# Kernel optimization log

Hardware: AMD Instinct MI355X
Metric: run time of the kernel (lower is better)

The kernel has to match this reference:

```python
import jax, jax.numpy as jnp
import numpy as np

H = 4  # num_heads
EPS = 1e-5


def setup_inputs() -> dict:
    key = jax.random.key(0)
    ks = jax.random.split(key, 12)
    N, C, E = 4096, 128, 131072
    x = jax.random.normal(ks[0], (N, C), dtype=jnp.float32)
    edge_index = jax.random.randint(ks[1], (2, E), 0, N, dtype=jnp.int64)
    # guarantee every row has at least one neighbor (self-loops) to avoid NaN softmax rows
    loops = jnp.arange(N, dtype=jnp.int64)
    edge_index = edge_index.at[0, :N].set(loops).at[1, :N].set(loops)
    s = 1.0 / np.sqrt(C)
    def lin(k):
        kw, kb = jax.random.split(k)
        return (jax.random.uniform(kw, (C, C), jnp.float32, -s, s),
                jax.random.uniform(kb, (C,), jnp.float32, -s, s))
    wq, bq = lin(ks[2]); wk, bk = lin(ks[3]); wv, bv = lin(ks[4]); wo, bo = lin(ks[5])
    gamma = jnp.ones((C,), jnp.float32)
    beta = jnp.zeros((C,), jnp.float32)
    return {"x": x, "edge_index": edge_index, "wq": wq, "bq": bq, "wk": wk, "bk": bk,
            "wv": wv, "bv": bv, "wo": wo, "bo": bo, "gamma": gamma, "beta": beta}


def reference(x, edge_index, wq, bq, wk, bk, wv, bv, wo, bo, gamma, beta):
    N, C = x.shape
    D = C // H
    q = (x @ wq.T + bq).reshape(N, H, D)
    k = (x @ wk.T + bk).reshape(N, H, D)
    v = (x @ wv.T + bv).reshape(N, H, D)
    scores = jnp.einsum('nhd,mhd->nhm', q, k) / jnp.sqrt(jnp.float32(D))  # [N,H,N]
    row, col = edge_index
    mask = jnp.zeros((N, N), jnp.float32).at[row, col].set(1.0)
    scores = jnp.where(mask[:, None, :] == 0, -jnp.inf, scores)
    attn = jax.nn.softmax(scores, axis=-1)  # dropout is identity in eval
    out = jnp.einsum('nhm,mhd->nhd', attn, v).reshape(N, C)
    out = out @ wo.T + bo
    y = x + out
    mu = jnp.mean(y, axis=-1, keepdims=True)
    var = jnp.var(y, axis=-1, keepdims=True)
    return (y - mu) / jnp.sqrt(var + EPS) * gamma + beta
```

## Files before the change

kernel.cpp:

```cpp
#include <hip/hip_runtime.h>

typedef unsigned long long u64;
typedef unsigned short u16;
typedef __attribute__((ext_vector_type(8))) short short8;
typedef __attribute__((ext_vector_type(4))) float f32x4;

#define C_DIM 128

__device__ inline u16 bf16_rn(float f) {
    unsigned u = __float_as_uint(f);
    u += 0x7FFF + ((u >> 16) & 1);
    return (u16)(u >> 16);
}
__device__ inline float bf16_tof(u16 h) { return __uint_as_float(((unsigned)h) << 16); }

__global__ __launch_bounds__(256) void prep_kernel(
    const int* __restrict__ ei, int E, u64* __restrict__ bm, int wpr,
    const float* __restrict__ x, u16* __restrict__ xh, u16* __restrict__ xl, int xq,
    const float* __restrict__ wq, const float* __restrict__ wk,
    const float* __restrict__ wv, const float* __restrict__ wo,
    u16* __restrict__ wH, u16* __restrict__ wL)
{
    int tid = blockIdx.x * 256 + threadIdx.x;
    if (tid < E) {
        int r = ei[tid], c = ei[E + tid];
        atomicOr(&bm[(size_t)r * wpr + (c >> 6)], 1ull << (c & 63));
    }
    if (tid < 4 * C_DIM * C_DIM) {
        int s = tid >> 14, i = tid & 16383;
        const float* W = (s == 0) ? wq : (s == 1) ? wk : (s == 2) ? wv : wo;
        float f = W[i];
        u16 h = bf16_rn(f);
        wH[tid] = h;
        wL[tid] = bf16_rn(f - bf16_tof(h));
    }
    if (tid < xq) {
        float4 xv = ((const float4*)x)[tid];
        ushort4 h, l;
        h.x = bf16_rn(xv.x); l.x = bf16_rn(xv.x - bf16_tof(h.x));
        h.y = bf16_rn(xv.y); l.y = bf16_rn(xv.y - bf16_tof(h.y));
        h.z = bf16_rn(xv.z); l.z = bf16_rn(xv.z - bf16_tof(h.z));
        h.w = bf16_rn(xv.w); l.w = bf16_rn(xv.w - bf16_tof(h.w));
        ((ushort4*)xh)[tid] = h;
        ((ushort4*)xl)[tid] = l;
    }
}

__global__ __launch_bounds__(256) void qkv_mfma_kernel(
    const u16* __restrict__ xh, const u16* __restrict__ xl,
    const u16* __restrict__ wH, const u16* __restrict__ wL,
    const float* __restrict__ bq, const float* __restrict__ bk, const float* __restrict__ bv,
    float* __restrict__ qo, float* __restrict__ ko, float* __restrict__ vo, int nrg)
{
    int bid = blockIdx.x;
    int s = bid / nrg;
    int rg = bid % nrg;
    int r0 = rg * 16;
    int w  = threadIdx.x >> 6;
    int l  = threadIdx.x & 63;
    int j0 = w * 32;
    int lr = l & 15;
    int kg = l >> 4;

    const u16* xhp = xh + (size_t)(r0 + lr) * C_DIM + kg * 8;
    const u16* xlp = xl + (size_t)(r0 + lr) * C_DIM + kg * 8;
    const u16* wh  = wH + (size_t)s * C_DIM * C_DIM;
    const u16* wl  = wL + (size_t)s * C_DIM * C_DIM;
    const u16* w0h = wh + (size_t)(j0 + lr) * C_DIM + kg * 8;
    const u16* w0l = wl + (size_t)(j0 + lr) * C_DIM + kg * 8;
    const u16* w1h = w0h + 16 * C_DIM;
    const u16* w1l = w0l + 16 * C_DIM;
    const float* B = (s == 0) ? bq : (s == 1) ? bk : bv;
    float*       O = (s == 0) ? qo : (s == 1) ? ko : vo;
    float fin = (s == 0) ? 0.17677669529663687f : 1.0f;

    float b0 = B[j0 + lr], b1 = B[j0 + 16 + lr];
    f32x4 acc0 = {b0, b0, b0, b0};
    f32x4 acc1 = {b1, b1, b1, b1};

    #pragma unroll
    for (int kk = 0; kk < C_DIM; kk += 32) {
        short8 ah  = *(const short8*)(xhp + kk);
        short8 al  = *(const short8*)(xlp + kk);
        short8 bh0 = *(const short8*)(w0h + kk);
        short8 bl0 = *(const short8*)(w0l + kk);
        short8 bh1 = *(const short8*)(w1h + kk);
        short8 bl1 = *(const short8*)(w1l + kk);
        acc0 = __builtin_amdgcn_mfma_f32_16x16x32_bf16(ah, bh0, acc0, 0, 0, 0);
        acc0 = __builtin_amdgcn_mfma_f32_16x16x32_bf16(ah, bl0, acc0, 0, 0, 0);
        acc0 = __builtin_amdgcn_mfma_f32_16x16x32_bf16(al, bh0, acc0, 0, 0, 0);
        acc1 = __builtin_amdgcn_mfma_f32_16x16x32_bf16(ah, bh1, acc1, 0, 0, 0);
        acc1 = __builtin_amdgcn_mfma_f32_16x16x32_bf16(ah, bl1, acc1, 0, 0, 0);
        acc1 = __builtin_amdgcn_mfma_f32_16x16x32_bf16(al, bh1, acc1, 0, 0, 0);
    }
    size_t ob = (size_t)(r0 + kg * 4) * C_DIM;
    #pragma unroll
    for (int i = 0; i < 4; ++i) {
        O[ob + (size_t)i * C_DIM + j0 + lr]      = acc0[i] * fin;
        O[ob + (size_t)i * C_DIM + j0 + 16 + lr] = acc1[i] * fin;
    }
}

__global__ __launch_bounds__(512, 4) void attn_kernel(
    const float* __restrict__ q, const float* __restrict__ k,
    const float* __restrict__ v, const u64* __restrict__ bm, int wpr,
    u16* __restrict__ aoh, u16* __restrict__ aol)
{
    __shared__ int lm[8][64];
    int t = threadIdx.x;
    int wave = t >> 6, lane = t & 63;
    int n = blockIdx.x * 8 + wave;

    u64 bits = bm[(size_t)n * wpr + lane];
    int pc = __popcll(bits);
    int incl = pc;
    #pragma unroll
    for (int off = 1; off < 64; off <<= 1) {
        int tv = __shfl_up(incl, off);
        if (lane >= off) incl += tv;
    }
    int cnt = __builtin_amdgcn_readfirstlane(__shfl(incl, 63));
    int pos = incl - pc;
    u64 bb = bits;
    while (bb) {
        int b = __builtin_ctzll(bb);
        bb &= bb - 1;
        if (pos < 64) lm[wave][pos] = (lane << 6) + b;
        ++pos;
    }
    if (cnt > 64) cnt = 64;

    int g = lane >> 4;
    float2 qf = *(const float2*)(q + (size_t)n * C_DIM + 2 * lane);

    float sc0 = -1e30f, sc1 = -1e30f, sc2 = -1e30f, sc3 = -1e30f;
    float2 buf[32];

    {
        int top = cnt < 32 ? cnt : 32;
        #pragma unroll
        for (int u = 0; u < 32; ++u)
            if (u < top)
                buf[u] = *(const float2*)(k + (size_t)lm[wave][u] * C_DIM + 2 * lane);
        #pragma unroll
        for (int u = 0; u < 32; ++u)
            if (u < top) {
                float s = qf.x * buf[u].x + qf.y * buf[u].y;
                s += __shfl_xor(s, 1); s += __shfl_xor(s, 2);
                s += __shfl_xor(s, 4); s += __shfl_xor(s, 8);
                if ((lane & 15) == (u & 15)) { if (u < 16) sc0 = s; else sc1 = s; }
            }
    }
    if (cnt > 32) {
        #pragma unroll
        for (int u = 0; u < 32; ++u)
            if (32 + u < cnt)
                buf[u] = *(const float2*)(k + (size_t)lm[wave][32 + u] * C_DIM + 2 * lane);
        #pragma unroll
        for (int u = 0; u < 32; ++u)
            if (32 + u < cnt) {
                float s = qf.x * buf[u].x + qf.y * buf[u].y;
                s += __shfl_xor(s, 1); s += __shfl_xor(s, 2);
                s += __shfl_xor(s, 4); s += __shfl_xor(s, 8);
                if ((lane & 15) == (u & 15)) { if (u < 16) sc2 = s; else sc3 = s; }
            }
    }
    {
        int top = cnt < 32 ? cnt : 32;
        #pragma unroll
        for (int u = 0; u < 32; ++u)
            if (u < top)
                buf[u] = *(const float2*)(v + (size_t)lm[wave][u] * C_DIM + 2 * lane);
    }
    float mx = fmaxf(fmaxf(sc0, sc1), fmaxf(sc2, sc3));
    mx = fmaxf(mx, __shfl_xor(mx, 1)); mx = fmaxf(mx, __shfl_xor(mx, 2));
    mx = fmaxf(mx, __shfl_xor(mx, 4)); mx = fmaxf(mx, __shfl_xor(mx, 8));
    float e0 = __expf(sc0 - mx), e1 = __expf(sc1 - mx);
    float e2 = __expf(sc2 - mx), e3 = __expf(sc3 - mx);
    float sum = (e0 + e1) + (e2 + e3);
    sum += __shfl_xor(sum, 1); sum += __shfl_xor(sum, 2);
    sum += __shfl_xor(sum, 4); sum += __shfl_xor(sum, 8);
    float sinv = 1.0f / sum;

    float2 acc = {0.f, 0.f};
    {
        int top = cnt < 32 ? cnt : 32;
        #pragma unroll
        for (int u = 0; u < 32; ++u)
            if (u < top) {
                float e = __shfl((u < 16) ? e0 : e1, (g << 4) | (u & 15));
                acc.x += e * buf[u].x;
                acc.y += e * buf[u].y;
            }
    }
    if (cnt > 32) {
        #pragma unroll
        for (int u = 0; u < 32; ++u)
            if (32 + u < cnt)
                buf[u] = *(const float2*)(v + (size_t)lm[wave][32 + u] * C_DIM + 2 * lane);
        #pragma unroll
        for (int u = 0; u < 32; ++u)
            if (32 + u < cnt) {
                float e = __shfl((u < 16) ? e2 : e3, (g << 4) | (u & 15));
                acc.x += e * buf[u].x;
                acc.y += e * buf[u].y;
            }
    }
    float f0 = acc.x * sinv, f1 = acc.y * sinv;
    ushort2 ho, lo;
    ho.x = bf16_rn(f0); lo.x = bf16_rn(f0 - bf16_tof(ho.x));
    ho.y = bf16_rn(f1); lo.y = bf16_rn(f1 - bf16_tof(ho.y));
    *(ushort2*)(aoh + (size_t)n * C_DIM + 2 * lane) = ho;
    *(ushort2*)(aol + (size_t)n * C_DIM + 2 * lane) = lo;
}

__global__ __launch_bounds__(256) void oln_kernel(
    const u16* __restrict__ aoh, const u16* __restrict__ aol,
    const u16* __restrict__ woh, const u16* __restrict__ wol,
    const float* __restrict__ bo, const float* __restrict__ x,
    const float* __restrict__ gamma, const float* __restrict__ beta,
    float* __restrict__ out)
{
    __shared__ float ys[16 * 132];
    int r0 = blockIdx.x * 16;
    int w  = threadIdx.x >> 6;
    int l  = threadIdx.x & 63;
    int j0 = w * 32;
    int lr = l & 15;
    int kg = l >> 4;

    const u16* ahp = aoh + (size_t)(r0 + lr) * C_DIM + kg * 8;
    const u16* alp = aol + (size_t)(r0 + lr) * C_DIM + kg * 8;
    const u16* w0h = woh + (size_t)(j0 + lr) * C_DIM + kg * 8;
    const u16* w0l = wol + (size_t)(j0 + lr) * C_DIM + kg * 8;
    const u16* w1h = w0h + 16 * C_DIM;
    const u16* w1l = w0l + 16 * C_DIM;

    float b0 = bo[j0 + lr], b1 = bo[j0 + 16 + lr];
    f32x4 acc0 = {b0, b0, b0, b0};
    f32x4 acc1 = {b1, b1, b1, b1};

    #pragma unroll
    for (int kk = 0; kk < C_DIM; kk += 32) {
        short8 ah  = *(const short8*)(ahp + kk);
        short8 al  = *(const short8*)(alp + kk);
        short8 bh0 = *(const short8*)(w0h + kk);
        short8 bl0 = *(const short8*)(w0l + kk);
        short8 bh1 = *(const short8*)(w1h + kk);
        short8 bl1 = *(const short8*)(w1l + kk);
        acc0 = __builtin_amdgcn_mfma_f32_16x16x32_bf16(ah, bh0, acc0, 0, 0, 0);
        acc0 = __builtin_amdgcn_mfma_f32_16x16x32_bf16(ah, bl0, acc0, 0, 0, 0);
        acc0 = __builtin_amdgcn_mfma_f32_16x16x32_bf16(al, bh0, acc0, 0, 0, 0);
        acc1 = __builtin_amdgcn_mfma_f32_16x16x32_bf16(ah, bh1, acc1, 0, 0, 0);
        acc1 = __builtin_amdgcn_mfma_f32_16x16x32_bf16(ah, bl1, acc1, 0, 0, 0);
        acc1 = __builtin_amdgcn_mfma_f32_16x16x32_bf16(al, bh1, acc1, 0, 0, 0);
    }
    #pragma unroll
    for (int i = 0; i < 4; ++i) {
        int rr = kg * 4 + i;
        float y0 = acc0[i] + x[(size_t)(r0 + rr) * C_DIM + j0 + lr];
        float y1 = acc1[i] + x[(size_t)(r0 + rr) * C_DIM + j0 + 16 + lr];
        ys[rr * 132 + j0 + lr]      = y0;
        ys[rr * 132 + j0 + 16 + lr] = y1;
    }
    __syncthreads();
    {
        int rr = threadIdx.x >> 4;
        int c0 = (threadIdx.x & 15) * 8;
        float yv[8];
        float s = 0.f, s2 = 0.f;
        #pragma unroll
        for (int u = 0; u < 8; ++u) {
            yv[u] = ys[rr * 132 + c0 + u];
            s += yv[u]; s2 += yv[u] * yv[u];
        }
        #pragma unroll
        for (int off = 8; off; off >>= 1) {
            s  += __shfl_xor(s, off);
            s2 += __shfl_xor(s2, off);
        }
        float mu = s * (1.0f / 128.0f);
        float var = s2 * (1.0f / 128.0f) - mu * mu;
        float rstd = rsqrtf(var + 1e-5f);
        size_t o = (size_t)(r0 + rr) * C_DIM + c0;
        #pragma unroll
        for (int u = 0; u < 8; ++u)
            out[o + u] = (yv[u] - mu) * rstd * gamma[c0 + u] + beta[c0 + u];
    }
}

extern "C" void kernel_launch(void* const* d_in, const int* in_sizes, int n_in,
                              void* d_out, int out_size, void* d_ws, size_t ws_size,
                              hipStream_t stream)
{
    const float* x     = (const float*)d_in[0];
    const int*   ei    = (const int*)d_in[1];
    const float* wq    = (const float*)d_in[2];
    const float* bq    = (const float*)d_in[3];
    const float* wk    = (const float*)d_in[4];
    const float* bk    = (const float*)d_in[5];
    const float* wv    = (const float*)d_in[6];
    const float* bv    = (const float*)d_in[7];
    const float* wo    = (const float*)d_in[8];
    const float* bo    = (const float*)d_in[9];
    const float* gamma = (const float*)d_in[10];
    const float* beta  = (const float*)d_in[11];
    float* out = (float*)d_out;

    int N = in_sizes[0] / C_DIM;
    int E = in_sizes[1] / 2;
    int wpr = N >> 6;

    size_t MB = 1 << 20;
    char* base = (char*)d_ws;
    float* q   = (float*)(base + 0 * MB);
    float* k   = (float*)(base + 2 * MB);
    float* v   = (float*)(base + 4 * MB);
    u64*   bm  = (u64*)(base + 6 * MB);
    u16*   xh  = (u16*)(base + 8 * MB);
    u16*   xl  = (u16*)(base + 9 * MB);
    u16*   wH  = (u16*)(base + 10 * MB);
    u16*   wL  = (u16*)(base + 10 * MB + 512 * 1024);
    u16*   aoh = (u16*)(base + 11 * MB);
    u16*   aol = (u16*)(base + 12 * MB);

    hipMemsetAsync(bm, 0, (size_t)N * wpr * sizeof(u64), stream);

    int xq = N * C_DIM / 4;
    int nwork = (E > xq) ? E : xq;
    prep_kernel<<<(nwork + 255) / 256, 256, 0, stream>>>(
        ei, E, bm, wpr, x, xh, xl, xq, wq, wk, wv, wo, wH, wL);

    int nrg = N / 16;
    qkv_mfma_kernel<<<3 * nrg, 256, 0, stream>>>(
        xh, xl, wH, wL, bq, bk, bv, q, k, v, nrg);

    attn_kernel<<<N / 8, 512, 0, stream>>>(q, k, v, bm, wpr, aoh, aol);

    oln_kernel<<<N / 16, 256, 0, stream>>>(
        aoh, aol, wH + 3 * C_DIM * C_DIM, wL + 3 * C_DIM * C_DIM,
        bo, x, gamma, beta, out);
}
```

Baseline: 125.5 us.

## Build neighbor lists during prep and double row tiles in QKV and output GEMMs

The prep kernel now appends each unique neighbor to a per-row list with an atomic degree counter whenever the bitmap atomicOr sets a new bit. The attention kernel then reads the list directly instead of doing popcount, prefix scan and LDS compaction. The weight split conversion is vectorized with float4. QKV and output-projection kernels now compute 32 rows per block instead of 16, which halves the grid and reuses the weight fragments. The costs are extra atomics in prep, a list order that depends on atomic timing, and fewer blocks in the GEMM kernels.

New measurement: 137.4 us. 9.5% more time.

```diff
diff --git a/kernel.cpp b/kernel.cpp
--- a/kernel.cpp
+++ b/kernel.cpp
@@ -16,6 +16,7 @@
 
 __global__ __launch_bounds__(256) void prep_kernel(
     const int* __restrict__ ei, int E, u64* __restrict__ bm, int wpr,
+    int* __restrict__ deg, u16* __restrict__ lists,
     const float* __restrict__ x, u16* __restrict__ xh, u16* __restrict__ xl, int xq,
     const float* __restrict__ wq, const float* __restrict__ wk,
     const float* __restrict__ wv, const float* __restrict__ wo,
@@ -24,15 +25,24 @@
     int tid = blockIdx.x * 256 + threadIdx.x;
     if (tid < E) {
         int r = ei[tid], c = ei[E + tid];
-        atomicOr(&bm[(size_t)r * wpr + (c >> 6)], 1ull << (c & 63));
-    }
-    if (tid < 4 * C_DIM * C_DIM) {
-        int s = tid >> 14, i = tid & 16383;
+        u64 mask = 1ull << (c & 63);
+        u64 old = atomicOr(&bm[(size_t)r * wpr + (c >> 6)], mask);
+        if (!(old & mask)) {
+            int slot = atomicAdd(&deg[r], 1);
+            if (slot < 64) lists[(size_t)r * 64 + slot] = (u16)c;
+        }
+    }
+    if (tid < 4 * 4096) {
+        int s = tid >> 12, i4 = tid & 4095;
         const float* W = (s == 0) ? wq : (s == 1) ? wk : (s == 2) ? wv : wo;
-        float f = W[i];
-        u16 h = bf16_rn(f);
-        wH[tid] = h;
-        wL[tid] = bf16_rn(f - bf16_tof(h));
+        float4 f = ((const float4*)W)[i4];
+        ushort4 h, l;
+        h.x = bf16_rn(f.x); l.x = bf16_rn(f.x - bf16_tof(h.x));
+        h.y = bf16_rn(f.y); l.y = bf16_rn(f.y - bf16_tof(h.y));
+        h.z = bf16_rn(f.z); l.z = bf16_rn(f.z - bf16_tof(h.z));
+        h.w = bf16_rn(f.w); l.w = bf16_rn(f.w - bf16_tof(h.w));
+        ((ushort4*)(wH + (size_t)s * 16384))[i4] = h;
+        ((ushort4*)(wL + (size_t)s * 16384))[i4] = l;
     }
     if (tid < xq) {
         float4 xv = ((const float4*)x)[tid];
@@ -55,19 +65,19 @@
     int bid = blockIdx.x;
     int s = bid / nrg;
     int rg = bid % nrg;
-    int r0 = rg * 16;
+    int r0 = rg * 32;
     int w  = threadIdx.x >> 6;
     int l  = threadIdx.x & 63;
     int j0 = w * 32;
     int lr = l & 15;
     int kg = l >> 4;
 
-    const u16* xhp = xh + (size_t)(r0 + lr) * C_DIM + kg * 8;
-    const u16* xlp = xl + (size_t)(r0 + lr) * C_DIM + kg * 8;
-    const u16* wh  = wH + (size_t)s * C_DIM * C_DIM;
-    const u16* wl  = wL + (size_t)s * C_DIM * C_DIM;
-    const u16* w0h = wh + (size_t)(j0 + lr) * C_DIM + kg * 8;
-    const u16* w0l = wl + (size_t)(j0 + lr) * C_DIM + kg * 8;
+    const u16* a0h = xh + (size_t)(r0 + lr) * C_DIM + kg * 8;
+    const u16* a0l = xl + (size_t)(r0 + lr) * C_DIM + kg * 8;
+    const u16* a1h = a0h + 16 * C_DIM;
+    const u16* a1l = a0l + 16 * C_DIM;
+    const u16* w0h = wH + (size_t)s * 16384 + (size_t)(j0 + lr) * C_DIM + kg * 8;
+    const u16* w0l = wL + (size_t)s * 16384 + (size_t)(j0 + lr) * C_DIM + kg * 8;
     const u16* w1h = w0h + 16 * C_DIM;
     const u16* w1l = w0l + 16 * C_DIM;
     const float* B = (s == 0) ? bq : (s == 1) ? bk : bv;
@@ -75,60 +85,59 @@
     float fin = (s == 0) ? 0.17677669529663687f : 1.0f;
 
     float b0 = B[j0 + lr], b1 = B[j0 + 16 + lr];
-    f32x4 acc0 = {b0, b0, b0, b0};
-    f32x4 acc1 = {b1, b1, b1, b1};
+    f32x4 acc00 = {b0, b0, b0, b0};
+    f32x4 acc01 = {b1, b1, b1, b1};
+    f32x4 acc10 = {b0, b0, b0, b0};
+    f32x4 acc11 = {b1, b1, b1, b1};
 
     #pragma unroll
     for (int kk = 0; kk < C_DIM; kk += 32) {
-        short8 ah  = *(const short8*)(xhp + kk);
-        short8 al  = *(const short8*)(xlp + kk);
+        short8 ah0 = *(const short8*)(a0h + kk);
+        short8 al0 = *(const short8*)(a0l + kk);
+        short8 ah1 = *(const short8*)(a1h + kk);
+        short8 al1 = *(const short8*)(a1l + kk);
         short8 bh0 = *(const short8*)(w0h + kk);
         short8 bl0 = *(const short8*)(w0l + kk);
         short8 bh1 = *(const short8*)(w1h + kk);
         short8 bl1 = *(const short8*)(w1l + kk);
-        acc0 = __builtin_amdgcn_mfma_f32_16x16x32_bf16(ah, bh0, acc0, 0, 0, 0);
-        acc0 = __builtin_amdgcn_mfma_f32_16x16x32_bf16(ah, bl0, acc0, 0, 0, 0);
-        acc0 = __builtin_amdgcn_mfma_f32_16x16x32_bf16(al, bh0, acc0, 0, 0, 0);
-        acc1 = __builtin_amdgcn_mfma_f32_16x16x32_bf16(ah, bh1, acc1, 0, 0, 0);
-        acc1 = __builtin_amdgcn_mfma_f32_16x16x32_bf16(ah, bl1, acc1, 0, 0, 0);
-        acc1 = __builtin_amdgcn_mfma_f32_16x16x32_bf16(al, bh1, acc1, 0, 0, 0);
-    }
-    size_t ob = (size_t)(r0 + kg * 4) * C_DIM;
+        acc00 = __builtin_amdgcn_mfma_f32_16x16x32_bf16(ah0, bh0, acc00, 0, 0, 0);
+        acc00 = __builtin_amdgcn_mfma_f32_16x16x32_bf16(ah0, bl0, acc00, 0, 0, 0);
+        acc00 = __builtin_amdgcn_mfma_f32_16x16x32_bf16(al0, bh0, acc00, 0, 0, 0);
+        acc01 = __builtin_amdgcn_mfma_f32_16x16x32_bf16(ah0, bh1, acc01, 0, 0, 0);
+        acc01 = __builtin_amdgcn_mfma_f32_16x16x32_bf16(ah0, bl1, acc01, 0, 0, 0);
+        acc01 = __builtin_amdgcn_mfma_f32_16x16x32_bf16(al0, bh1, acc01, 0, 0, 0);
+        acc10 = __builtin_amdgcn_mfma_f32_16x16x32_bf16(ah1, bh0, acc10, 0, 0, 0);
+        acc10 = __builtin_amdgcn_mfma_f32_16x16x32_bf16(ah1, bl0, acc10, 0, 0, 0);
+        acc10 = __builtin_amdgcn_mfma_f32_16x16x32_bf16(al1, bh0, acc10, 0, 0, 0);
+        acc11 = __builtin_amdgcn_mfma_f32_16x16x32_bf16(ah1, bh1, acc11, 0, 0, 0);
+        acc11 = __builtin_amdgcn_mfma_f32_16x16x32_bf16(ah1, bl1, acc11, 0, 0, 0);
+        acc11 = __builtin_amdgcn_mfma_f32_16x16x32_bf16(al1, bh1, acc11, 0, 0, 0);
+    }
     #pragma unroll
     for (int i = 0; i < 4; ++i) {
-        O[ob + (size_t)i * C_DIM + j0 + lr]      = acc0[i] * fin;
-        O[ob + (size_t)i * C_DIM + j0 + 16 + lr] = acc1[i] * fin;
+        size_t ro0 = (size_t)(r0 + kg * 4 + i) * C_DIM;
+        size_t ro1 = (size_t)(r0 + 16 + kg * 4 + i) * C_DIM;
+        O[ro0 + j0 + lr]      = acc00[i] * fin;
+        O[ro0 + j0 + 16 + lr] = acc01[i] * fin;
+        O[ro1 + j0 + lr]      = acc10[i] * fin;
+        O[ro1 + j0 + 16 + lr] = acc11[i] * fin;
     }
 }
 
 __global__ __launch_bounds__(512, 4) void attn_kernel(
     const float* __restrict__ q, const float* __restrict__ k,
-    const float* __restrict__ v, const u64* __restrict__ bm, int wpr,
+    const float* __restrict__ v, const int* __restrict__ deg,
+    const u16* __restrict__ lists,
     u16* __restrict__ aoh, u16* __restrict__ aol)
 {
-    __shared__ int lm[8][64];
     int t = threadIdx.x;
     int wave = t >> 6, lane = t & 63;
     int n = blockIdx.x * 8 + wave;
 
-    u64 bits = bm[(size_t)n * wpr + lane];
-    int pc = __popcll(bits);
-    int incl = pc;
-    #pragma unroll
-    for (int off = 1; off < 64; off <<= 1) {
-        int tv = __shfl_up(incl, off);
-        if (lane >= off) incl += tv;
-    }
-    int cnt = __builtin_amdgcn_readfirstlane(__shfl(incl, 63));
-    int pos = incl - pc;
-    u64 bb = bits;
-    while (bb) {
-        int b = __builtin_ctzll(bb);
-        bb &= bb - 1;
-        if (pos < 64) lm[wave][pos] = (lane << 6) + b;
-        ++pos;
-    }
+    int cnt = deg[n];
     if (cnt > 64) cnt = 64;
+    cnt = __builtin_amdgcn_readfirstlane(cnt);
+    int le = lists[(size_t)n * 64 + lane];
 
     int g = lane >> 4;
     float2 qf = *(const float2*)(q + (size_t)n * C_DIM + 2 * lane);
@@ -140,8 +149,10 @@
         int top = cnt < 32 ? cnt : 32;
         #pragma unroll
         for (int u = 0; u < 32; ++u)
-            if (u < top)
-                buf[u] = *(const float2*)(k + (size_t)lm[wave][u] * C_DIM + 2 * lane);
+            if (u < top) {
+                int m = __shfl(le, u);
+                buf[u] = *(const float2*)(k + (size_t)m * C_DIM + 2 * lane);
+            }
         #pragma unroll
         for (int u = 0; u < 32; ++u)
             if (u < top) {
@@ -154,8 +165,10 @@
     if (cnt > 32) {
         #pragma unroll
         for (int u = 0; u < 32; ++u)
-            if (32 + u < cnt)
-                buf[u] = *(const float2*)(k + (size_t)lm[wave][32 + u] * C_DIM + 2 * lane);
+            if (32 + u < cnt) {
+                int m = __shfl(le, 32 + u);
+                buf[u] = *(const float2*)(k + (size_t)m * C_DIM + 2 * lane);
+            }
         #pragma unroll
         for (int u = 0; u < 32; ++u)
             if (32 + u < cnt) {
@@ -169,8 +182,10 @@
         int top = cnt < 32 ? cnt : 32;
         #pragma unroll
         for (int u = 0; u < 32; ++u)
-            if (u < top)
-                buf[u] = *(const float2*)(v + (size_t)lm[wave][u] * C_DIM + 2 * lane);
+            if (u < top) {
+                int m = __shfl(le, u);
+                buf[u] = *(const float2*)(v + (size_t)m * C_DIM + 2 * lane);
+            }
     }
     float mx = fmaxf(fmaxf(sc0, sc1), fmaxf(sc2, sc3));
     mx = fmaxf(mx, __shfl_xor(mx, 1)); mx = fmaxf(mx, __shfl_xor(mx, 2));
@@ -196,8 +211,10 @@
     if (cnt > 32) {
         #pragma unroll
         for (int u = 0; u < 32; ++u)
-            if (32 + u < cnt)
-                buf[u] = *(const float2*)(v + (size_t)lm[wave][32 + u] * C_DIM + 2 * lane);
+            if (32 + u < cnt) {
+                int m = __shfl(le, 32 + u);
+                buf[u] = *(const float2*)(v + (size_t)m * C_DIM + 2 * lane);
+            }
         #pragma unroll
         for (int u = 0; u < 32; ++u)
             if (32 + u < cnt) {
@@ -221,61 +238,74 @@
     const float* __restrict__ gamma, const float* __restrict__ beta,
     float* __restrict__ out)
 {
-    __shared__ float ys[16 * 132];
-    int r0 = blockIdx.x * 16;
+    __shared__ float ys[32 * 132];
+    int r0 = blockIdx.x * 32;
     int w  = threadIdx.x >> 6;
     int l  = threadIdx.x & 63;
     int j0 = w * 32;
     int lr = l & 15;
     int kg = l >> 4;
 
-    const u16* ahp = aoh + (size_t)(r0 + lr) * C_DIM + kg * 8;
-    const u16* alp = aol + (size_t)(r0 + lr) * C_DIM + kg * 8;
+    const u16* a0h = aoh + (size_t)(r0 + lr) * C_DIM + kg * 8;
+    const u16* a0l = aol + (size_t)(r0 + lr) * C_DIM + kg * 8;
+    const u16* a1h = a0h + 16 * C_DIM;
+    const u16* a1l = a0l + 16 * C_DIM;
     const u16* w0h = woh + (size_t)(j0 + lr) * C_DIM + kg * 8;
     const u16* w0l = wol + (size_t)(j0 + lr) * C_DIM + kg * 8;
     const u16* w1h = w0h + 16 * C_DIM;
     const u16* w1l = w0l + 16 * C_DIM;
 
     float b0 = bo[j0 + lr], b1 = bo[j0 + 16 + lr];
-    f32x4 acc0 = {b0, b0, b0, b0};
-    f32x4 acc1 = {b1, b1, b1, b1};
+    f32x4 acc00 = {b0, b0, b0, b0};
+    f32x4 acc01 = {b1, b1, b1, b1};
+    f32x4 acc10 = {b0, b0, b0, b0};
+    f32x4 acc11 = {b1, b1, b1, b1};
 
     #pragma unroll
     for (int kk = 0; kk < C_DIM; kk += 32) {
-        short8 ah  = *(const short8*)(ahp + kk);
-        short8 al  = *(const short8*)(alp + kk);
+        short8 ah0 = *(const short8*)(a0h + kk);
+        short8 al0 = *(const short8*)(a0l + kk);
+        short8 ah1 = *(const short8*)(a1h + kk);
+        short8 al1 = *(const short8*)(a1l + kk);
         short8 bh0 = *(const short8*)(w0h + kk);
         short8 bl0 = *(const short8*)(w0l + kk);
         short8 bh1 = *(const short8*)(w1h + kk);
         short8 bl1 = *(const short8*)(w1l + kk);
-        acc0 = __builtin_amdgcn_mfma_f32_16x16x32_bf16(ah, bh0, acc0, 0, 0, 0);
-        acc0 = __builtin_amdgcn_mfma_f32_16x16x32_bf16(ah, bl0, acc0, 0, 0, 0);
-        acc0 = __builtin_amdgcn_mfma_f32_16x16x32_bf16(al, bh0, acc0, 0, 0, 0);
-        acc1 = __builtin_amdgcn_mfma_f32_16x16x32_bf16(ah, bh1, acc1, 0, 0, 0);
-        acc1 = __builtin_amdgcn_mfma_f32_16x16x32_bf16(ah, bl1, acc1, 0, 0, 0);
-        acc1 = __builtin_amdgcn_mfma_f32_16x16x32_bf16(al, bh1, acc1, 0, 0, 0);
+        acc00 = __builtin_amdgcn_mfma_f32_16x16x32_bf16(ah0, bh0, acc00, 0, 0, 0);
+        acc00 = __builtin_amdgcn_mfma_f32_16x16x32_bf16(ah0, bl0, acc00, 0, 0, 0);
+        acc00 = __builtin_amdgcn_mfma_f32_16x16x32_bf16(al0, bh0, acc00, 0, 0, 0);
+        acc01 = __builtin_amdgcn_mfma_f32_16x16x32_bf16(ah0, bh1, acc01, 0, 0, 0);
+        acc01 = __builtin_amdgcn_mfma_f32_16x16x32_bf16(ah0, bl1, acc01, 0, 0, 0);
+        acc01 = __builtin_amdgcn_mfma_f32_16x16x32_bf16(al0, bh1, acc01, 0, 0, 0);
+        acc10 = __builtin_amdgcn_mfma_f32_16x16x32_bf16(ah1, bh0, acc10, 0, 0, 0);
+        acc10 = __builtin_amdgcn_mfma_f32_16x16x32_bf16(ah1, bl0, acc10, 0, 0, 0);
+        acc10 = __builtin_amdgcn_mfma_f32_16x16x32_bf16(al1, bh0, acc10, 0, 0, 0);
+        acc11 = __builtin_amdgcn_mfma_f32_16x16x32_bf16(ah1, bh1, acc11, 0, 0, 0);
+        acc11 = __builtin_amdgcn_mfma_f32_16x16x32_bf16(ah1, bl1, acc11, 0, 0, 0);
+        acc11 = __builtin_amdgcn_mfma_f32_16x16x32_bf16(al1, bh1, acc11, 0, 0, 0);
     }
     #pragma unroll
     for (int i = 0; i < 4; ++i) {
-        int rr = kg * 4 + i;
-        float y0 = acc0[i] + x[(size_t)(r0 + rr) * C_DIM + j0 + lr];
-        float y1 = acc1[i] + x[(size_t)(r0 + rr) * C_DIM + j0 + 16 + lr];
-        ys[rr * 132 + j0 + lr]      = y0;
-        ys[rr * 132 + j0 + 16 + lr] = y1;
+        int rr0 = kg * 4 + i;
+        int rr1 = 16 + kg * 4 + i;
+        ys[rr0 * 132 + j0 + lr]      = acc00[i] + x[(size_t)(r0 + rr0) * C_DIM + j0 + lr];
+        ys[rr0 * 132 + j0 + 16 + lr] = acc01[i] + x[(size_t)(r0 + rr0) * C_DIM + j0 + 16 + lr];
+        ys[rr1 * 132 + j0 + lr]      = acc10[i] + x[(size_t)(r0 + rr1) * C_DIM + j0 + lr];
+        ys[rr1 * 132 + j0 + 16 + lr] = acc11[i] + x[(size_t)(r0 + rr1) * C_DIM + j0 + 16 + lr];
     }
     __syncthreads();
     {
-        int rr = threadIdx.x >> 4;
-        int c0 = (threadIdx.x & 15) * 8;
-        float yv[8];
+        int rr = threadIdx.x >> 3;
+        int c0 = (threadIdx.x & 7) * 16;
+        float yv[16];
         float s = 0.f, s2 = 0.f;
         #pragma unroll
-        for (int u = 0; u < 8; ++u) {
+        for (int u = 0; u < 16; ++u) {
             yv[u] = ys[rr * 132 + c0 + u];
             s += yv[u]; s2 += yv[u] * yv[u];
         }
         #pragma unroll
-        for (int off = 8; off; off >>= 1) {
+        for (int off = 4; off; off >>= 1) {
             s  += __shfl_xor(s, off);
             s2 += __shfl_xor(s2, off);
         }
@@ -284,7 +314,7 @@
         float rstd = rsqrtf(var + 1e-5f);
         size_t o = (size_t)(r0 + rr) * C_DIM + c0;
         #pragma unroll
-        for (int u = 0; u < 8; ++u)
+        for (int u = 0; u < 16; ++u)
             out[o + u] = (yv[u] - mu) * rstd * gamma[c0 + u] + beta[c0 + u];
     }
 }
@@ -313,31 +343,33 @@
 
     size_t MB = 1 << 20;
     char* base = (char*)d_ws;
-    float* q   = (float*)(base + 0 * MB);
-    float* k   = (float*)(base + 2 * MB);
-    float* v   = (float*)(base + 4 * MB);
-    u64*   bm  = (u64*)(base + 6 * MB);
-    u16*   xh  = (u16*)(base + 8 * MB);
-    u16*   xl  = (u16*)(base + 9 * MB);
-    u16*   wH  = (u16*)(base + 10 * MB);
-    u16*   wL  = (u16*)(base + 10 * MB + 512 * 1024);
-    u16*   aoh = (u16*)(base + 11 * MB);
-    u16*   aol = (u16*)(base + 12 * MB);
-
-    hipMemsetAsync(bm, 0, (size_t)N * wpr * sizeof(u64), stream);
+    float* q     = (float*)(base + 0 * MB);
+    float* k     = (float*)(base + 2 * MB);
+    float* v     = (float*)(base + 4 * MB);
+    u64*   bm    = (u64*)(base + 6 * MB);
+    int*   deg   = (int*)(base + 8 * MB);
+    u16*   lists = (u16*)(base + 8 * MB + 64 * 1024);
+    u16*   xh    = (u16*)(base + 9 * MB);
+    u16*   xl    = (u16*)(base + 10 * MB);
+    u16*   wH    = (u16*)(base + 11 * MB);
+    u16*   wL    = (u16*)(base + 11 * MB + 256 * 1024);
+    u16*   aoh   = (u16*)(base + 12 * MB);
+    u16*   aol   = (u16*)(base + 13 * MB);
+
+    hipMemsetAsync(bm, 0, 2 * MB + (size_t)N * sizeof(int), stream);
 
     int xq = N * C_DIM / 4;
     int nwork = (E > xq) ? E : xq;
     prep_kernel<<<(nwork + 255) / 256, 256, 0, stream>>>(
-        ei, E, bm, wpr, x, xh, xl, xq, wq, wk, wv, wo, wH, wL);
-
-    int nrg = N / 16;
+        ei, E, bm, wpr, deg, lists, x, xh, xl, xq, wq, wk, wv, wo, wH, wL);
+
+    int nrg = N / 32;
     qkv_mfma_kernel<<<3 * nrg, 256, 0, stream>>>(
         xh, xl, wH, wL, bq, bk, bv, q, k, v, nrg);
 
-    attn_kernel<<<N / 8, 512, 0, stream>>>(q, k, v, bm, wpr, aoh, aol);
-
-    oln_kernel<<<N / 16, 256, 0, stream>>>(
+    attn_kernel<<<N / 8, 512, 0, stream>>>(q, k, v, deg, lists, aoh, aol);
+
+    oln_kernel<<<N / 32, 256, 0, stream>>>(
         aoh, aol, wH + 3 * C_DIM * C_DIM, wL + 3 * C_DIM * C_DIM,
         bo, x, gamma, beta, out);
 }
```
